# Performance work log

Measured on AMD Instinct MI355X. Metric: run time of the kernel, lower is better.

## Reference

```python
import jax, jax.numpy as jnp
import numpy as np


def setup_inputs() -> dict:
    key = jax.random.key(0)
    ks = jax.random.split(key, 9)
    B, C, H, W = 16, 64, 256, 256  # N == C is required by GCN.conv1d_1
    p = lambda k, shape: jax.random.normal(k, shape, dtype=jnp.float32) * 0.05
    return {
        "x": jax.random.normal(ks[0], (B, C, H, W), dtype=jnp.float32),
        "theta_w": p(ks[1], (C, C)),   # Conv2d(C, N=C, 1) weight, squeezed to [N, C]
        "theta_b": p(ks[2], (C,)),
        "g1_w": p(ks[3], (C, C)),      # Conv1d(N, N, 1) weight, squeezed to [N, N]
        "g1_b": p(ks[4], (C,)),
        "g2_w": p(ks[5], (1, 1)),      # Conv1d(1, 1, 1) weight
        "g2_b": p(ks[6], (1,)),
        "phi_w": p(ks[7], (C,)),       # Conv2d(1, C, 1) weight, squeezed to [C]
        "phi_b": p(ks[8], (C,)),
    }


def reference(x, theta_w, theta_b, g1_w, g1_b, g2_w, g2_b, phi_w, phi_b):
    # x: [B, C, H, W], with N == C and mid_channels == 1
    # AdaptiveAvgPool2d(1): global average pool -> node features [B, C]
    x_node = jnp.mean(x, axis=(2, 3))
    # theta: 1x1 Conv2d C -> N, kept as 4D map [B, N, H, W]
    Bmap = jnp.einsum('nc,bchw->bnhw', theta_w, x) + theta_b[None, :, None, None]
    # GCN: conv1d_1 (1x1 over length-1 sequence) == dense matmul on channels
    h = x_node @ g1_w.T + g1_b                      # [B, N]
    # permute -> [B, 1, N]; conv1d_2 on the single channel is scalar affine
    z1 = h * g2_w[0, 0] + g2_b[0]                   # [B, N]
    # B^T @ z1 : contract node dim, producing the 1-channel spatial map y
    y = jnp.einsum('bnhw,bn->bhw', Bmap, z1)[:, None]  # [B, 1, H, W]
    # phi_inv: 1x1 Conv2d 1 -> C (broadcast multiply + bias)
    x_res = y * phi_w[None, :, None, None] + phi_b[None, :, None, None]
    # self.sigmoid is actually nn.Tanh()
    return jnp.tanh(x_res + x)
```

## Files before the change

### kernel.cpp

```cpp
#include <hip/hip_runtime.h>
#include <hip/hip_bf16.h>

#define B_   16
#define C_   64
#define HW_  65536

typedef float    f2_t __attribute__((ext_vector_type(2)));
typedef float    f4_t __attribute__((ext_vector_type(4)));
typedef _Float16 h2_t __attribute__((ext_vector_type(2)));
typedef _Float16 h4_t __attribute__((ext_vector_type(4)));

__device__ __forceinline__ float fast_tanh(float z) {
    z = fminf(fmaxf(z, -15.f), 15.f);
    float e = __expf(2.f * z);
    return 1.f - 2.f * __builtin_amdgcn_rcpf(e + 1.f);
}

__global__ __launch_bounds__(256) void k_reduce_compress(
    const float* __restrict__ x, float* __restrict__ x_node,
    h4_t* __restrict__ xh) {
    int bc  = blockIdx.x;
    int tid = threadIdx.x;
    const f4_t* p4 = (const f4_t*)(x + (size_t)bc * HW_);
    h4_t* oh = xh + (size_t)bc * (HW_ / 4);

    float s = 0.f;
#pragma unroll
    for (int i = 0; i < 64; ++i) {
        f4_t v = __builtin_nontemporal_load(p4 + tid + 256 * i);
        s += (v.x + v.y) + (v.z + v.w);
        h4_t h;
        h.x = (_Float16)v.x; h.y = (_Float16)v.y;
        h.z = (_Float16)v.z; h.w = (_Float16)v.w;
        oh[tid + 256 * i] = h;
    }
#pragma unroll
    for (int off = 32; off; off >>= 1) s += __shfl_down(s, off, 64);

    __shared__ float ls[4];
    int wid = tid >> 6, lane = tid & 63;
    if (lane == 0) ls[wid] = s;
    __syncthreads();
    if (tid == 0) {
        float t = (ls[0] + ls[1]) + (ls[2] + ls[3]);
        x_node[bc] = t * (1.0f / (float)HW_);
    }
}

__global__ __launch_bounds__(256) void k_fused_h(
    const _Float16* __restrict__ xh, const float* __restrict__ x_node,
    const float* __restrict__ theta_w, const float* __restrict__ theta_b,
    const float* __restrict__ g1_w,    const float* __restrict__ g1_b,
    const float* __restrict__ g2_w,    const float* __restrict__ g2_b,
    const float* __restrict__ phi_w,   const float* __restrict__ phi_b,
    float* __restrict__ out) {
    __shared__ float xn[C_], z1[C_], wsh[C_], pw[C_], pb[C_];
    __shared__ float hp[4][C_];
    __shared__ float bias_s;

    int t = threadIdx.x;
    int b = blockIdx.x >> 7;
    int chunk = 127 - (blockIdx.x & 127);
    int pix = (chunk * 256 + t) * 2;

    int n = t & 63, q = t >> 6;
    if (t < C_) { xn[t] = x_node[b * C_ + t]; pw[t] = phi_w[t]; pb[t] = phi_b[t]; }
    __syncthreads();
    float hpart = 0.f;
#pragma unroll
    for (int i = 0; i < 16; ++i) {
        int c = q * 16 + i;
        hpart += xn[c] * g1_w[n * C_ + c];
    }
    hp[q][n] = hpart;
    __syncthreads();
    if (t < C_) {
        float h = g1_b[t] + (hp[0][t] + hp[1][t]) + (hp[2][t] + hp[3][t]);
        z1[t] = h * g2_w[0] + g2_b[0];
    }
    __syncthreads();
    float wpart = 0.f;
#pragma unroll
    for (int i = 0; i < 16; ++i) {
        int nn = q * 16 + i;
        wpart += z1[nn] * theta_w[nn * C_ + n];
    }
    hp[q][n] = wpart;
    if (t == 0) {
        float bb = 0.f;
#pragma unroll
        for (int nn = 0; nn < C_; ++nn) bb += z1[nn] * theta_b[nn];
        bias_s = bb;
    }
    __syncthreads();
    if (t < C_) wsh[t] = (hp[0][t] + hp[1][t]) + (hp[2][t] + hp[3][t]);
    __syncthreads();

    const h2_t* xb = (const h2_t*)(xh + (size_t)b * C_ * HW_ + pix);

    h2_t xs[C_];
    float y0 = bias_s;
    float y1 = y0;
#pragma unroll
    for (int c = 0; c < C_; ++c) {
        h2_t v = xb[c * (HW_ / 2)];
        xs[c] = v;
        float w = wsh[c];
        y0 += w * (float)v.x;
        y1 += w * (float)v.y;
    }

    float* ob = out + (size_t)b * C_ * HW_ + pix;
#pragma unroll
    for (int c = 0; c < C_; ++c) {
        float a = pw[c], d = pb[c];
        f2_t r;
        r.x = fast_tanh(y0 * a + d + (float)xs[c].x);
        r.y = fast_tanh(y1 * a + d + (float)xs[c].y);
        __builtin_nontemporal_store(r, (f2_t*)(ob + (size_t)c * HW_));
    }
}

__global__ __launch_bounds__(256) void k_reduce_mean(
    const float* __restrict__ x, float* __restrict__ x_node) {
    int bc  = blockIdx.x;
    int tid = threadIdx.x;
    const float4* p4 = (const float4*)(x + (size_t)bc * HW_);
    float s = 0.f;
#pragma unroll
    for (int i = 0; i < 64; ++i) {
        float4 v = p4[tid + 256 * i];
        s += (v.x + v.y) + (v.z + v.w);
    }
#pragma unroll
    for (int off = 32; off; off >>= 1) s += __shfl_down(s, off, 64);
    __shared__ float ls[4];
    int wid = tid >> 6, lane = tid & 63;
    if (lane == 0) ls[wid] = s;
    __syncthreads();
    if (tid == 0)
        x_node[bc] = ((ls[0] + ls[1]) + (ls[2] + ls[3])) * (1.0f / (float)HW_);
}

__global__ __launch_bounds__(256) void k_fused_reg(
    const float* __restrict__ x, const float* __restrict__ x_node,
    const float* __restrict__ theta_w, const float* __restrict__ theta_b,
    const float* __restrict__ g1_w,    const float* __restrict__ g1_b,
    const float* __restrict__ g2_w,    const float* __restrict__ g2_b,
    const float* __restrict__ phi_w,   const float* __restrict__ phi_b,
    float* __restrict__ out) {
    __shared__ float xn[C_], z1[C_], wsh[C_], pw[C_], pb[C_];
    __shared__ float hp[4][C_];
    __shared__ float bias_s;

    int t = threadIdx.x;
    int b = blockIdx.x >> 7;
    int chunk = 127 - (blockIdx.x & 127);
    int pix = (chunk * 256 + t) * 2;

    int n = t & 63, q = t >> 6;
    if (t < C_) { xn[t] = x_node[b * C_ + t]; pw[t] = phi_w[t]; pb[t] = phi_b[t]; }
    __syncthreads();
    float hpart = 0.f;
#pragma unroll
    for (int i = 0; i < 16; ++i) {
        int c = q * 16 + i;
        hpart += xn[c] * g1_w[n * C_ + c];
    }
    hp[q][n] = hpart;
    __syncthreads();
    if (t < C_) {
        float h = g1_b[t] + (hp[0][t] + hp[1][t]) + (hp[2][t] + hp[3][t]);
        z1[t] = h * g2_w[0] + g2_b[0];
    }
    __syncthreads();
    float wpart = 0.f;
#pragma unroll
    for (int i = 0; i < 16; ++i) {
        int nn = q * 16 + i;
        wpart += z1[nn] * theta_w[nn * C_ + n];
    }
    hp[q][n] = wpart;
    if (t == 0) {
        float bb = 0.f;
#pragma unroll
        for (int nn = 0; nn < C_; ++nn) bb += z1[nn] * theta_b[nn];
        bias_s = bb;
    }
    __syncthreads();
    if (t < C_) wsh[t] = (hp[0][t] + hp[1][t]) + (hp[2][t] + hp[3][t]);
    __syncthreads();

    const float* xb = x + (size_t)b * C_ * HW_ + pix;
    f2_t xs[C_];
    float y0 = bias_s;
    float y1 = y0;
#pragma unroll
    for (int c = 0; c < C_; ++c) {
        f2_t v = *(const f2_t*)(xb + (size_t)c * HW_);
        xs[c] = v;
        float w = wsh[c];
        y0 += w * v.x;
        y1 += w * v.y;
    }
    float* ob = out + (size_t)b * C_ * HW_ + pix;
#pragma unroll
    for (int c = 0; c < C_; ++c) {
        float a = pw[c], d = pb[c];
        f2_t r;
        r.x = fast_tanh(y0 * a + d + xs[c].x);
        r.y = fast_tanh(y1 * a + d + xs[c].y);
        __builtin_nontemporal_store(r, (f2_t*)(ob + (size_t)c * HW_));
    }
}

extern "C" void kernel_launch(void* const* d_in, const int* in_sizes, int n_in,
                              void* d_out, int out_size, void* d_ws, size_t ws_size,
                              hipStream_t stream) {
    const float* x       = (const float*)d_in[0];
    const float* theta_w = (const float*)d_in[1];
    const float* theta_b = (const float*)d_in[2];
    const float* g1_w    = (const float*)d_in[3];
    const float* g1_b    = (const float*)d_in[4];
    const float* g2_w    = (const float*)d_in[5];
    const float* g2_b    = (const float*)d_in[6];
    const float* phi_w   = (const float*)d_in[7];
    const float* phi_b   = (const float*)d_in[8];
    float* out = (float*)d_out;

    float* x_node = (float*)d_ws;
    const size_t xh_off   = 4096;
    const size_t xh_bytes = (size_t)B_ * C_ * HW_ * sizeof(_Float16);

    if (ws_size >= xh_off + xh_bytes) {
        _Float16* xh = (_Float16*)((char*)d_ws + xh_off);
        k_reduce_compress<<<B_ * C_, 256, 0, stream>>>(x, x_node, (h4_t*)xh);
        k_fused_h<<<B_ * (HW_ / 512), 256, 0, stream>>>(
            xh, x_node, theta_w, theta_b, g1_w, g1_b, g2_w, g2_b,
            phi_w, phi_b, out);
    } else {
        k_reduce_mean<<<B_ * C_, 256, 0, stream>>>(x, x_node);
        k_fused_reg<<<B_ * (HW_ / 512), 256, 0, stream>>>(
            x, x_node, theta_w, theta_b, g1_w, g1_b, g2_w, g2_b,
            phi_w, phi_b, out);
    }
}
```

Before: 131.1 us.

## Replace two-pass fp16 staging with persistent cooperative kernel using grid sync

```diff
diff --git a/kernel.cpp b/kernel.cpp
--- a/kernel.cpp
+++ b/kernel.cpp
@@ -1,14 +1,17 @@
 #include <hip/hip_runtime.h>
-#include <hip/hip_bf16.h>
+#include <hip/hip_cooperative_groups.h>
+
+namespace cg = cooperative_groups;
 
 #define B_   16
 #define C_   64
 #define HW_  65536
+#define GRP  8
+#define NBLK 1024
+#define NTHR 256
 
 typedef float    f2_t __attribute__((ext_vector_type(2)));
-typedef float    f4_t __attribute__((ext_vector_type(4)));
 typedef _Float16 h2_t __attribute__((ext_vector_type(2)));
-typedef _Float16 h4_t __attribute__((ext_vector_type(4)));
 
 __device__ __forceinline__ float fast_tanh(float z) {
     z = fminf(fmaxf(z, -15.f), 15.f);
@@ -16,108 +19,133 @@
     return 1.f - 2.f * __builtin_amdgcn_rcpf(e + 1.f);
 }
 
-__global__ __launch_bounds__(256) void k_reduce_compress(
-    const float* __restrict__ x, float* __restrict__ x_node,
-    h4_t* __restrict__ xh) {
-    int bc  = blockIdx.x;
-    int tid = threadIdx.x;
-    const f4_t* p4 = (const f4_t*)(x + (size_t)bc * HW_);
-    h4_t* oh = xh + (size_t)bc * (HW_ / 4);
-
-    float s = 0.f;
-#pragma unroll
-    for (int i = 0; i < 64; ++i) {
-        f4_t v = __builtin_nontemporal_load(p4 + tid + 256 * i);
-        s += (v.x + v.y) + (v.z + v.w);
-        h4_t h;
-        h.x = (_Float16)v.x; h.y = (_Float16)v.y;
-        h.z = (_Float16)v.z; h.w = (_Float16)v.w;
-        oh[tid + 256 * i] = h;
-    }
-#pragma unroll
-    for (int off = 32; off; off >>= 1) s += __shfl_down(s, off, 64);
-
-    __shared__ float ls[4];
-    int wid = tid >> 6, lane = tid & 63;
-    if (lane == 0) ls[wid] = s;
-    __syncthreads();
-    if (tid == 0) {
-        float t = (ls[0] + ls[1]) + (ls[2] + ls[3]);
-        x_node[bc] = t * (1.0f / (float)HW_);
-    }
-}
-
-__global__ __launch_bounds__(256) void k_fused_h(
-    const _Float16* __restrict__ xh, const float* __restrict__ x_node,
+__global__ __launch_bounds__(NTHR, 4) void k_persist(
+    const float* __restrict__ x,
     const float* __restrict__ theta_w, const float* __restrict__ theta_b,
     const float* __restrict__ g1_w,    const float* __restrict__ g1_b,
     const float* __restrict__ g2_w,    const float* __restrict__ g2_b,
     const float* __restrict__ phi_w,   const float* __restrict__ phi_b,
-    float* __restrict__ out) {
+    float* __restrict__ gsums, float* __restrict__ out) {
+
+    cg::grid_group grid = cg::this_grid();
+    int t    = threadIdx.x;
+    int bi   = blockIdx.x >> 7;
+    int pix  = ((blockIdx.x & 127) * NTHR + t) * 2;
+    int lane = t & 63, wid = t >> 6;
+
+    __shared__ float wsum[4][C_];
     __shared__ float xn[C_], z1[C_], wsh[C_], pw[C_], pb[C_];
     __shared__ float hp[4][C_];
     __shared__ float bias_s;
 
-    int t = threadIdx.x;
-    int b = blockIdx.x >> 7;
-    int chunk = 127 - (blockIdx.x & 127);
-    int pix = (chunk * 256 + t) * 2;
-
-    int n = t & 63, q = t >> 6;
-    if (t < C_) { xn[t] = x_node[b * C_ + t]; pw[t] = phi_w[t]; pb[t] = phi_b[t]; }
-    __syncthreads();
-    float hpart = 0.f;
-#pragma unroll
-    for (int i = 0; i < 16; ++i) {
-        int c = q * 16 + i;
-        hpart += xn[c] * g1_w[n * C_ + c];
-    }
-    hp[q][n] = hpart;
-    __syncthreads();
-    if (t < C_) {
-        float h = g1_b[t] + (hp[0][t] + hp[1][t]) + (hp[2][t] + hp[3][t]);
-        z1[t] = h * g2_w[0] + g2_b[0];
-    }
-    __syncthreads();
-    float wpart = 0.f;
-#pragma unroll
-    for (int i = 0; i < 16; ++i) {
-        int nn = q * 16 + i;
-        wpart += z1[nn] * theta_w[nn * C_ + n];
-    }
-    hp[q][n] = wpart;
-    if (t == 0) {
-        float bb = 0.f;
-#pragma unroll
-        for (int nn = 0; nn < C_; ++nn) bb += z1[nn] * theta_b[nn];
-        bias_s = bb;
-    }
-    __syncthreads();
-    if (t < C_) wsh[t] = (hp[0][t] + hp[1][t]) + (hp[2][t] + hp[3][t]);
-    __syncthreads();
-
-    const h2_t* xb = (const h2_t*)(xh + (size_t)b * C_ * HW_ + pix);
+    if (t < C_) { pw[t] = phi_w[t]; pb[t] = phi_b[t]; }
+    float g2w0 = g2_w[0], g2b0 = g2_b[0];
 
     h2_t xs[C_];
-    float y0 = bias_s;
-    float y1 = y0;
-#pragma unroll
-    for (int c = 0; c < C_; ++c) {
-        h2_t v = xb[c * (HW_ / 2)];
-        xs[c] = v;
-        float w = wsh[c];
-        y0 += w * (float)v.x;
-        y1 += w * (float)v.y;
-    }
-
-    float* ob = out + (size_t)b * C_ * HW_ + pix;
-#pragma unroll
-    for (int c = 0; c < C_; ++c) {
-        float a = pw[c], d = pb[c];
-        f2_t r;
-        r.x = fast_tanh(y0 * a + d + (float)xs[c].x);
-        r.y = fast_tanh(y1 * a + d + (float)xs[c].y);
-        __builtin_nontemporal_store(r, (f2_t*)(ob + (size_t)c * HW_));
+
+    for (int g = 0; g < 2; ++g) {
+        int b = g * GRP + bi;
+        const float* xb = x + (size_t)b * C_ * HW_ + pix;
+
+#pragma unroll
+        for (int k = 0; k < 8; ++k) {
+            float pt[8];
+#pragma unroll
+            for (int i = 0; i < 8; ++i) {
+                int c = k * 8 + i;
+                f2_t v = *(const f2_t*)(xb + (size_t)c * HW_);
+                h2_t h; h.x = (_Float16)v.x; h.y = (_Float16)v.y;
+                xs[c] = h;
+                pt[i] = v.x + v.y;
+            }
+            {
+                bool hi = (lane & 32) != 0;
+                float a0 = hi ? pt[4] : pt[0], s0 = hi ? pt[0] : pt[4];
+                float a1 = hi ? pt[5] : pt[1], s1 = hi ? pt[1] : pt[5];
+                float a2 = hi ? pt[6] : pt[2], s2 = hi ? pt[2] : pt[6];
+                float a3 = hi ? pt[7] : pt[3], s3 = hi ? pt[3] : pt[7];
+                pt[0] = a0 + __shfl_xor(s0, 32, 64);
+                pt[1] = a1 + __shfl_xor(s1, 32, 64);
+                pt[2] = a2 + __shfl_xor(s2, 32, 64);
+                pt[3] = a3 + __shfl_xor(s3, 32, 64);
+            }
+            {
+                bool hi = (lane & 16) != 0;
+                float a0 = hi ? pt[2] : pt[0], s0 = hi ? pt[0] : pt[2];
+                float a1 = hi ? pt[3] : pt[1], s1 = hi ? pt[1] : pt[3];
+                pt[0] = a0 + __shfl_xor(s0, 16, 64);
+                pt[1] = a1 + __shfl_xor(s1, 16, 64);
+            }
+            float q;
+            {
+                bool hi = (lane & 8) != 0;
+                float a = hi ? pt[1] : pt[0], s = hi ? pt[0] : pt[1];
+                q = a + __shfl_xor(s, 8, 64);
+            }
+            q += __shfl_xor(q, 4, 64);
+            q += __shfl_xor(q, 2, 64);
+            q += __shfl_xor(q, 1, 64);
+            if ((lane & 7) == 0)
+                wsum[wid][k * 8 + ((lane >> 3) & 7)] = q;
+        }
+        __syncthreads();
+        if (t < C_) {
+            float gs = (wsum[0][t] + wsum[1][t]) + (wsum[2][t] + wsum[3][t]);
+            atomicAdd(&gsums[b * C_ + t], gs);
+        }
+
+        grid.sync();
+
+        int n = t & 63, q4 = t >> 6;
+        if (t < C_) xn[t] = gsums[b * C_ + t] * (1.0f / (float)HW_);
+        __syncthreads();
+        float hpart = 0.f;
+#pragma unroll
+        for (int i = 0; i < 16; ++i) {
+            int c = q4 * 16 + i;
+            hpart += xn[c] * g1_w[n * C_ + c];
+        }
+        hp[q4][n] = hpart;
+        __syncthreads();
+        if (t < C_) {
+            float h = g1_b[t] + (hp[0][t] + hp[1][t]) + (hp[2][t] + hp[3][t]);
+            z1[t] = h * g2w0 + g2b0;
+        }
+        __syncthreads();
+        float wpart = 0.f;
+#pragma unroll
+        for (int i = 0; i < 16; ++i) {
+            int nn = q4 * 16 + i;
+            wpart += z1[nn] * theta_w[nn * C_ + n];
+        }
+        hp[q4][n] = wpart;
+        if (t == 0) {
+            float bb = 0.f;
+#pragma unroll
+            for (int nn = 0; nn < C_; ++nn) bb += z1[nn] * theta_b[nn];
+            bias_s = bb;
+        }
+        __syncthreads();
+        if (t < C_) wsh[t] = (hp[0][t] + hp[1][t]) + (hp[2][t] + hp[3][t]);
+        __syncthreads();
+
+        float y0 = bias_s, y1 = bias_s;
+#pragma unroll
+        for (int c = 0; c < C_; ++c) {
+            float w = wsh[c];
+            y0 += w * (float)xs[c].x;
+            y1 += w * (float)xs[c].y;
+        }
+        float* ob = out + (size_t)b * C_ * HW_ + pix;
+#pragma unroll
+        for (int c = 0; c < C_; ++c) {
+            float a = pw[c], d = pb[c];
+            f2_t r;
+            r.x = fast_tanh(y0 * a + d + (float)xs[c].x);
+            r.y = fast_tanh(y1 * a + d + (float)xs[c].y);
+            __builtin_nontemporal_store(r, (f2_t*)(ob + (size_t)c * HW_));
+        }
+        __syncthreads();
     }
 }
 
@@ -193,8 +221,7 @@
 
     const float* xb = x + (size_t)b * C_ * HW_ + pix;
     f2_t xs[C_];
-    float y0 = bias_s;
-    float y1 = y0;
+    float y0 = bias_s, y1 = bias_s;
 #pragma unroll
     for (int c = 0; c < C_; ++c) {
         f2_t v = *(const f2_t*)(xb + (size_t)c * HW_);
@@ -228,17 +255,19 @@
     const float* phi_b   = (const float*)d_in[8];
     float* out = (float*)d_out;
 
-    float* x_node = (float*)d_ws;
-    const size_t xh_off   = 4096;
-    const size_t xh_bytes = (size_t)B_ * C_ * HW_ * sizeof(_Float16);
-
-    if (ws_size >= xh_off + xh_bytes) {
-        _Float16* xh = (_Float16*)((char*)d_ws + xh_off);
-        k_reduce_compress<<<B_ * C_, 256, 0, stream>>>(x, x_node, (h4_t*)xh);
-        k_fused_h<<<B_ * (HW_ / 512), 256, 0, stream>>>(
-            xh, x_node, theta_w, theta_b, g1_w, g1_b, g2_w, g2_b,
-            phi_w, phi_b, out);
-    } else {
+    float* gsums  = (float*)d_ws;
+    float* x_node = gsums + B_ * C_;
+
+    hipMemsetAsync(gsums, 0, B_ * C_ * sizeof(float), stream);
+
+    void* args[] = {
+        (void*)&x, (void*)&theta_w, (void*)&theta_b,
+        (void*)&g1_w, (void*)&g1_b, (void*)&g2_w, (void*)&g2_b,
+        (void*)&phi_w, (void*)&phi_b, (void*)&gsums, (void*)&out
+    };
+    hipError_t err = hipLaunchCooperativeKernel((void*)k_persist, dim3(NBLK),
+                                                dim3(NTHR), args, 0, stream);
+    if (err != hipSuccess) {
         k_reduce_mean<<<B_ * C_, 256, 0, stream>>>(x, x_node);
         k_fused_reg<<<B_ * (HW_ / 512), 256, 0, stream>>>(
             x, x_node, theta_w, theta_b, g1_w, g1_b, g2_w, g2_b,
```

New measurement: 442.9 us. 3.38x slower.
